# Kernel tuning notes

Measured on AMD Instinct MI355X. Metric: run time of the kernel, lower is better.

Reference implementation:

```python
import jax, jax.numpy as jnp
import numpy as np

EPS_BN = 1e-5
EPS_NORM = 1e-12
NUM_HEADS = 8


def _bn_relu(x):
    # BatchNorm2d in training mode with fresh params (gamma=1, beta=0), then ReLU.
    m = x.mean((0, 2, 3), keepdims=True)
    v = x.var((0, 2, 3), keepdims=True)  # biased variance, as PyTorch uses for normalization
    return jax.nn.relu((x - m) * jax.lax.rsqrt(v + EPS_BN))


def _conv3(x, w, groups=1):
    # 3x3 conv, stride 1, padding 1 (NCHW / OIHW)
    return jax.lax.conv_general_dilated(
        x, w, (1, 1), ((1, 1), (1, 1)),
        dimension_numbers=('NCHW', 'OIHW', 'NCHW'),
        feature_group_count=groups)


def _encoder(x, w1, w2, w3):
    # Conv1x1 -> BN -> ReLU -> Conv k2 s2 -> BN -> ReLU -> Conv1x1 -> BN -> ReLU
    x = _bn_relu(jnp.einsum('bihw,oi->bohw', x, w1))
    b, c, h, w = x.shape
    # k=2,s=2 conv as a reshape + einsum (non-overlapping 2x2 patches)
    x = _bn_relu(jnp.einsum('bchpwq,ocpq->bohw', x.reshape(b, c, h // 2, 2, w // 2, 2), w2))
    return _bn_relu(jnp.einsum('bihw,oi->bohw', x, w3))


def _decoder(x, w1, w2, w3):
    # ConvT1x1 -> BN -> ReLU -> ConvT k2 s2 -> BN -> ReLU -> ConvT1x1 -> BN -> ReLU
    x = _bn_relu(jnp.einsum('bihw,io->bohw', x, w1))
    # ConvTranspose k=2,s=2: each input pixel expands to a 2x2 block
    y = jnp.einsum('bihw,iopq->bohpwq', x, w2)
    b, o, h, p, w, q = y.shape
    x = _bn_relu(y.reshape(b, o, h * p, w * q))
    return _bn_relu(jnp.einsum('bihw,io->bohw', x, w3))


def _l2norm(x):
    # F.normalize(dim=-1) with eps=1e-12
    return x / jnp.maximum(jnp.linalg.norm(x, axis=-1, keepdims=True), EPS_NORM)


def setup_inputs() -> dict:
    key = jax.random.key(0)
    ks = jax.random.split(key, 13)
    B, C, H, W = 8, 256, 64, 64
    d = C // 4  # attention dim after self.divide

    def rn(k, shape, s=0.1):
        return jax.random.normal(k, shape, jnp.float32) * s

    return {
        'x': jax.random.normal(ks[0], (B, C, H, W), jnp.float32),
        'y': jax.random.normal(ks[1], (B, C, H, W), jnp.float32),
        'temperature': jnp.ones((NUM_HEADS, 1, 1), jnp.float32),
        'enc_w1': rn(ks[2], (d // 2, C)),
        'enc_w2': rn(ks[3], (d // 2, d // 2, 2, 2)),
        'enc_w3': rn(ks[4], (d, d // 2)),
        'kv_w': rn(ks[5], (2 * d, d)),
        'kv_dw_w': rn(ks[6], (2 * d, 1, 3, 3)),
        'q_w': rn(ks[7], (d, d)),
        'q_dw_w': rn(ks[8], (d, d, 3, 3)),
        'proj_w': rn(ks[9], (d, d)),
        'dec_w1': rn(ks[10], (d, 2 * d)),
        'dec_w2': rn(ks[11], (2 * d, 2 * d, 2, 2)),
        'dec_w3': rn(ks[12], (2 * d, 4 * d)),
    }


def reference(x, y, temperature, enc_w1, enc_w2, enc_w3, kv_w, kv_dw_w,
              q_w, q_dw_w, proj_w, dec_w1, dec_w2, dec_w3):
    # Shared freshly-built encoder applied to both x and y (same weights,
    # BN batch stats computed per call).
    x = _encoder(x, enc_w1, enc_w2, enc_w3)
    y = _encoder(y, enc_w1, enc_w2, enc_w3)
    b, c, h, w = x.shape  # c = 64, h = w = 32

    kv = _conv3(jnp.einsum('bihw,oi->bohw', x, kv_w), kv_dw_w, groups=2 * c)
    k, v = jnp.split(kv, 2, axis=1)
    q = _conv3(jnp.einsum('bihw,oi->bohw', y, q_w), q_dw_w)  # regular 3x3 conv

    ch = c // NUM_HEADS
    heads = lambda t: t.reshape(b, NUM_HEADS, ch, h * w)  # b head c (h w)
    q, k, v = heads(q), heads(k), heads(v)
    q = _l2norm(q)
    k = _l2norm(k)
    temp = temperature[None]  # [1, head, 1, 1]

    # Spatial attention: [b, head, hw, hw]
    attn_s = jax.nn.softmax(jnp.einsum('bhcn,bhcm->bhnm', q, k) * temp, axis=-1)
    out_s = jnp.einsum('bhcn,bhnm->bhcm', v, attn_s).reshape(b, c, h, w)
    out_s = jnp.einsum('bihw,oi->bohw', out_s, proj_w)

    # Channel attention: [b, head, c, c]
    attn_c = jax.nn.softmax(jnp.einsum('bhcn,bhdn->bhcd', q, k) * temp, axis=-1)
    out_c = jnp.einsum('bhcd,bhdn->bhcn', attn_c, v).reshape(b, c, h, w)
    out_c = jnp.einsum('bihw,oi->bohw', out_c, proj_w)

    return _decoder(out_s + out_c, dec_w1, dec_w2, dec_w3)
```

## Files before the change

kernel.cpp:

```cpp
#include <hip/hip_runtime.h>
#include <hip/hip_bf16.h>

#define EPS_BN 1e-5f

#define PIPE_FENCE() asm volatile("" ::: "memory")

template<int OT, bool HASBN, bool HASSTATS>
__global__ __launch_bounds__(256,2) void conv1x1_kernel(
    const float* __restrict__ in0, const float* __restrict__ in1,
    const float* __restrict__ w, float* __restrict__ out,
    const float* __restrict__ stIn, float* __restrict__ stOut,
    int I, int O, int P, int wio, int zsplit, float invN)
{
  __shared__ float wl[2048];
  __shared__ float bnm[256], bnr[256];
  int tid = threadIdx.x;
  int o0 = blockIdx.y*OT;
  int z  = blockIdx.z;
  int t  = (z >= zsplit) ? 1 : 0;
  int b  = t ? (z - zsplit) : z;
  const float* in = t ? in1 : in0;

  for(int idx=tid; idx<I*OT; idx+=256){
    int i = idx/OT, j = idx - i*OT;
    wl[idx] = wio ? w[(size_t)i*O + o0 + j] : w[(size_t)(o0+j)*I + i];
  }
  if(HASBN){
    for(int i=tid; i<I; i+=256){
      float s  = stIn[((size_t)t*I + i)*2];
      float s2 = stIn[((size_t)t*I + i)*2+1];
      float m  = s*invN;
      bnm[i] = m;
      bnr[i] = rsqrtf(s2*invN - m*m + EPS_BN);
    }
  }
  __syncthreads();

  int p4 = blockIdx.x*256 + tid;
  const float4* inb = (const float4*)(in + (size_t)b*I*P) + p4;
  int P4 = P >> 2;

  float acc[OT][4];
#pragma unroll
  for(int j=0;j<OT;j++){ acc[j][0]=acc[j][1]=acc[j][2]=acc[j][3]=0.f; }

  auto consume = [&](const float4* vv, int i0){
#pragma unroll
    for(int u=0;u<8;u++){
      float4 v = vv[u];
      if(HASBN){
        float m = bnm[i0+u], r = bnr[i0+u];
        v.x = fmaxf((v.x-m)*r, 0.f); v.y = fmaxf((v.y-m)*r, 0.f);
        v.z = fmaxf((v.z-m)*r, 0.f); v.w = fmaxf((v.w-m)*r, 0.f);
      }
      const float* wr = &wl[(i0+u)*OT];
#pragma unroll
      for(int j=0;j<OT;j++){
        float wv = wr[j];
        acc[j][0] = fmaf(wv, v.x, acc[j][0]);
        acc[j][1] = fmaf(wv, v.y, acc[j][1]);
        acc[j][2] = fmaf(wv, v.z, acc[j][2]);
        acc[j][3] = fmaf(wv, v.w, acc[j][3]);
      }
    }
  };

  float4 va[8], vb[8];
#pragma unroll
  for(int u=0;u<8;u++) va[u] = inb[(size_t)u*P4];
  PIPE_FENCE();

  for(int i0=0;i0<I;i0+=16){
#pragma unroll
    for(int u=0;u<8;u++) vb[u] = inb[(size_t)(i0+8+u)*P4];
    PIPE_FENCE();
    consume(va, i0);
    if(i0+16 < I){
#pragma unroll
      for(int u=0;u<8;u++) va[u] = inb[(size_t)(i0+16+u)*P4];
    }
    PIPE_FENCE();
    consume(vb, i0+8);
  }

  float4* ob = (float4*)(out + ((size_t)z*O + o0)*P) + p4;
#pragma unroll
  for(int j=0;j<OT;j++){
    float4 vv = {acc[j][0], acc[j][1], acc[j][2], acc[j][3]};
    ob[(size_t)j*P4] = vv;
  }

  if(HASSTATS){
#pragma unroll
    for(int j=0;j<OT;j++){
      float s  = acc[j][0]+acc[j][1]+acc[j][2]+acc[j][3];
      float s2 = acc[j][0]*acc[j][0]+acc[j][1]*acc[j][1]
               + acc[j][2]*acc[j][2]+acc[j][3]*acc[j][3];
      for(int off=32; off>0; off>>=1){
        s  += __shfl_down(s,  off, 64);
        s2 += __shfl_down(s2, off, 64);
      }
      if((tid & 63)==0){
        atomicAdd(&stOut[((size_t)t*O + o0 + j)*2],   s);
        atomicAdd(&stOut[((size_t)t*O + o0 + j)*2+1], s2);
      }
    }
  }
}

template<int OT, bool HASBN, bool HASSTATS>
__global__ __launch_bounds__(256) void conv1x1_small(
    const float* __restrict__ in0, const float* __restrict__ in1,
    const float* __restrict__ w, float* __restrict__ out,
    const float* __restrict__ stIn, float* __restrict__ stOut,
    int I, int O, int wio, int zsplit, float invN)
{
  __shared__ float wl[512];
  __shared__ float bnm[128], bnr[128];
  int tid = threadIdx.x;
  int z  = blockIdx.z;
  int t  = (z >= zsplit) ? 1 : 0;
  int b  = t ? (z - zsplit) : z;
  const float* in = t ? in1 : in0;
  int W2 = 2*OT;

  for(int idx=tid; idx<I*W2; idx+=256){
    int i = idx/W2, slot = idx - i*W2;
    int oabs = blockIdx.y*W2 + slot;
    wl[idx] = wio ? w[(size_t)i*O + oabs] : w[(size_t)oabs*I + i];
  }
  if(HASBN){
    for(int i=tid; i<I; i+=256){
      float s  = stIn[((size_t)t*I + i)*2];
      float s2 = stIn[((size_t)t*I + i)*2+1];
      float m  = s*invN;
      bnm[i] = m;
      bnr[i] = rsqrtf(s2*invN - m*m + EPS_BN);
    }
  }
  __syncthreads();

  int p4 = blockIdx.x*128 + (tid & 127);
  int os = tid >> 7;
  const float4* inb = (const float4*)(in + (size_t)b*I*1024) + p4;

  float acc[OT][4];
#pragma unroll
  for(int j=0;j<OT;j++){ acc[j][0]=acc[j][1]=acc[j][2]=acc[j][3]=0.f; }

  float4 vb[8];
  for(int i0=0;i0<I;i0+=8){
#pragma unroll
    for(int u=0;u<8;u++) vb[u] = inb[(size_t)(i0+u)*256];
    PIPE_FENCE();
#pragma unroll
    for(int u=0;u<8;u++){
      float4 v = vb[u];
      if(HASBN){
        float m = bnm[i0+u], r = bnr[i0+u];
        v.x = fmaxf((v.x-m)*r, 0.f); v.y = fmaxf((v.y-m)*r, 0.f);
        v.z = fmaxf((v.z-m)*r, 0.f); v.w = fmaxf((v.w-m)*r, 0.f);
      }
      const float* wr = &wl[(i0+u)*W2 + os*OT];
#pragma unroll
      for(int j=0;j<OT;j++){
        float wv = wr[j];
        acc[j][0] = fmaf(wv, v.x, acc[j][0]);
        acc[j][1] = fmaf(wv, v.y, acc[j][1]);
        acc[j][2] = fmaf(wv, v.z, acc[j][2]);
        acc[j][3] = fmaf(wv, v.w, acc[j][3]);
      }
    }
  }

  int obase = blockIdx.y*W2 + os*OT;
  float4* ob = (float4*)(out + ((size_t)z*O + obase)*1024) + p4;
#pragma unroll
  for(int j=0;j<OT;j++){
    float4 vv = {acc[j][0], acc[j][1], acc[j][2], acc[j][3]};
    ob[(size_t)j*256] = vv;
  }

  if(HASSTATS){
#pragma unroll
    for(int j=0;j<OT;j++){
      float s  = acc[j][0]+acc[j][1]+acc[j][2]+acc[j][3];
      float s2 = acc[j][0]*acc[j][0]+acc[j][1]*acc[j][1]
               + acc[j][2]*acc[j][2]+acc[j][3]*acc[j][3];
      for(int off=32; off>0; off>>=1){
        s  += __shfl_down(s,  off, 64);
        s2 += __shfl_down(s2, off, 64);
      }
      if((tid & 63)==0){
        atomicAdd(&stOut[((size_t)t*O + obase + j)*2],   s);
        atomicAdd(&stOut[((size_t)t*O + obase + j)*2+1], s2);
      }
    }
  }
}

__global__ __launch_bounds__(256) void conv2x2s2_bn_kernel(
    const float* __restrict__ in, const float* __restrict__ w,
    float* __restrict__ out, const float* __restrict__ stIn,
    float* __restrict__ stOut, float invN)
{
  __shared__ float wl[512];
  __shared__ float bnm[32], bnr[32];
  int tid = threadIdx.x;
  int o0 = blockIdx.x*4;
  int rq = blockIdx.y;
  int z  = blockIdx.z;
  int t  = z >> 3;

  for(int idx=tid; idx<512; idx+=256){
    int osub = idx>>7, ch=(idx>>2)&31, pq=idx&3;
    wl[idx] = w[(((size_t)(o0+osub)*32 + ch)*4) + pq];
  }
  if(tid < 32){
    float s  = stIn[((size_t)t*32 + tid)*2];
    float s2 = stIn[((size_t)t*32 + tid)*2+1];
    float m  = s*invN;
    bnm[tid] = m;
    bnr[tid] = rsqrtf(s2*invN - m*m + EPS_BN);
  }
  __syncthreads();

  int os   = tid >> 6;
  int slot = tid & 63;
  int h    = rq*8 + (slot>>3);
  int wg   = slot & 7;
  int cb   = wg*8;
  const float* wbase = &wl[os*128];
  const float* inz = in + (size_t)z*32*4096;

  float acc[4] = {0,0,0,0};
  float4 c0,c1,c2,c3, n0_,n1_,n2_,n3_;
  c0 = *(const float4*)(inz + (size_t)0*4096 + (2*h)*64 + cb);
  c1 = *(const float4*)(inz + (size_t)0*4096 + (2*h)*64 + cb + 4);
  c2 = *(const float4*)(inz + (size_t)0*4096 + (2*h+1)*64 + cb);
  c3 = *(const float4*)(inz + (size_t)0*4096 + (2*h+1)*64 + cb + 4);
  for(int ch=0; ch<32; ch++){
    if(ch < 31){
      n0_ = *(const float4*)(inz + (size_t)(ch+1)*4096 + (2*h)*64 + cb);
      n1_ = *(const float4*)(inz + (size_t)(ch+1)*4096 + (2*h)*64 + cb + 4);
      n2_ = *(const float4*)(inz + (size_t)(ch+1)*4096 + (2*h+1)*64 + cb);
      n3_ = *(const float4*)(inz + (size_t)(ch+1)*4096 + (2*h+1)*64 + cb + 4);
    }
    float m = bnm[ch], r = bnr[ch];
    float t0[8] = {c0.x,c0.y,c0.z,c0.w,c1.x,c1.y,c1.z,c1.w};
    float t1[8] = {c2.x,c2.y,c2.z,c2.w,c3.x,c3.y,c3.z,c3.w};
#pragma unroll
    for(int e=0;e<8;e++){
      t0[e] = fmaxf((t0[e]-m)*r, 0.f);
      t1[e] = fmaxf((t1[e]-m)*r, 0.f);
    }
    const float* wp = wbase + ch*4;
#pragma unroll
    for(int k=0;k<4;k++){
      acc[k] = fmaf(wp[0], t0[2*k],   acc[k]);
      acc[k] = fmaf(wp[1], t0[2*k+1], acc[k]);
      acc[k] = fmaf(wp[2], t1[2*k],   acc[k]);
      acc[k] = fmaf(wp[3], t1[2*k+1], acc[k]);
    }
    c0=n0_; c1=n1_; c2=n2_; c3=n3_;
  }

  float4 vv = {acc[0],acc[1],acc[2],acc[3]};
  *(float4*)(out + ((size_t)z*32 + o0+os)*1024 + h*32 + wg*4) = vv;

  float s  = acc[0]+acc[1]+acc[2]+acc[3];
  float s2 = acc[0]*acc[0]+acc[1]*acc[1]+acc[2]*acc[2]+acc[3]*acc[3];
  for(int off=32; off>0; off>>=1){
    s  += __shfl_down(s,  off, 64);
    s2 += __shfl_down(s2, off, 64);
  }
  if((tid & 63)==0){
    atomicAdd(&stOut[((size_t)t*32 + o0 + os)*2],   s);
    atomicAdd(&stOut[((size_t)t*32 + o0 + os)*2+1], s2);
  }
}

__global__ __launch_bounds__(256) void upsample2x2_bn_kernel(
    const float* __restrict__ in, const float* __restrict__ w,
    float* __restrict__ out, const float* __restrict__ stIn,
    float* __restrict__ stOut, float invN)
{
  __shared__ float wl[1024];
  __shared__ float bnm[128], bnr[128];
  int tid = threadIdx.x;
  int o0 = blockIdx.x*2;
  int b  = blockIdx.y;

  for(int idx=tid; idx<1024; idx+=256){
    int pq = idx & 3, r = idx >> 2;
    int i = r >> 1, j = r & 1;
    wl[idx] = w[((size_t)i*128 + o0+j)*4 + pq];
  }
  if(tid < 128){
    float s  = stIn[(size_t)tid*2];
    float s2 = stIn[(size_t)tid*2+1];
    float m  = s*invN;
    bnm[tid] = m;
    bnr[tid] = rsqrtf(s2*invN - m*m + EPS_BN);
  }
  __syncthreads();

  int h  = tid >> 3;
  int wg = tid & 7;
  int w0 = wg*4;

  float acc[2][16];
#pragma unroll
  for(int j=0;j<2;j++) for(int e=0;e<16;e++) acc[j][e]=0.f;

  float4 vb4[8];
  for(int i0=0;i0<128;i0+=8){
#pragma unroll
    for(int u=0;u<8;u++)
      vb4[u] = *(const float4*)(in + (((size_t)b*128+i0+u)*1024) + h*32 + w0);
    PIPE_FENCE();
#pragma unroll
    for(int u=0;u<8;u++){
      int i = i0+u;
      float4 v = vb4[u];
      float m = bnm[i], r = bnr[i];
      float vk[4] = {fmaxf((v.x-m)*r,0.f), fmaxf((v.y-m)*r,0.f),
                     fmaxf((v.z-m)*r,0.f), fmaxf((v.w-m)*r,0.f)};
#pragma unroll
      for(int j=0;j<2;j++){
        const float* wj = &wl[(i*2+j)*4];
#pragma unroll
        for(int pq=0;pq<4;pq++){
#pragma unroll
          for(int k=0;k<4;k++)
            acc[j][pq*4+k] = fmaf(wj[pq], vk[k], acc[j][pq*4+k]);
        }
      }
    }
  }

#pragma unroll
  for(int j=0;j<2;j++){
    float* ob = out + ((size_t)b*128 + o0+j)*4096;
#pragma unroll
    for(int p=0;p<2;p++){
      float4 A = {acc[j][(p*2+0)*4+0], acc[j][(p*2+1)*4+0],
                  acc[j][(p*2+0)*4+1], acc[j][(p*2+1)*4+1]};
      float4 B = {acc[j][(p*2+0)*4+2], acc[j][(p*2+1)*4+2],
                  acc[j][(p*2+0)*4+3], acc[j][(p*2+1)*4+3]};
      *(float4*)(ob + (2*h+p)*64 + 2*w0)     = A;
      *(float4*)(ob + (2*h+p)*64 + 2*w0 + 4) = B;
    }
  }

#pragma unroll
  for(int j=0;j<2;j++){
    float s=0.f, s2=0.f;
#pragma unroll
    for(int e=0;e<16;e++){ s += acc[j][e]; s2 += acc[j][e]*acc[j][e]; }
    for(int off=32; off>0; off>>=1){
      s  += __shfl_down(s,  off, 64);
      s2 += __shfl_down(s2, off, 64);
    }
    if((tid & 63)==0){
      atomicAdd(&stOut[((size_t)(o0+j))*2],   s);
      atomicAdd(&stOut[((size_t)(o0+j))*2+1], s2);
    }
  }
}

__global__ __launch_bounds__(256) void bn_final_kernel(
    float* __restrict__ x, const float* __restrict__ st, float invN)
{
  int idx4 = blockIdx.x*256 + threadIdx.x;
  int c = (idx4 >> 10) & 255;
  float s  = st[(size_t)c*2];
  float s2 = st[(size_t)c*2+1];
  float m  = s*invN;
  float r  = rsqrtf(s2*invN - m*m + EPS_BN);
  float4 v = ((float4*)x)[idx4];
  v.x = fmaxf((v.x-m)*r, 0.f); v.y = fmaxf((v.y-m)*r, 0.f);
  v.z = fmaxf((v.z-m)*r, 0.f); v.w = fmaxf((v.w-m)*r, 0.f);
  ((float4*)x)[idx4] = v;
}

__global__ __launch_bounds__(256) void dwconv3x3_kernel(
    const float* __restrict__ in, const float* __restrict__ w,
    float* __restrict__ out, int C)
{
  int c = blockIdx.x, b = blockIdx.y;
  int tid = threadIdx.x;
  __shared__ float wl[9];
  if(tid < 9) wl[tid] = w[c*9 + tid];
  __syncthreads();
  int h = tid >> 3, x4 = tid & 7;
  int c0 = x4*4;
  const float* base = in + ((size_t)b*C + c)*1024;
  float ax=0.f, ay=0.f, az=0.f, aw=0.f;
#pragma unroll
  for(int dr=0; dr<3; dr++){
    int r = h + dr - 1;
    if((unsigned)r >= 32u) continue;
    const float* row = base + r*32 + c0;
    float4 cc = *(const float4*)row;
    float l  = (x4>0) ? row[-1] : 0.f;
    float rr = (x4<7) ? row[4]  : 0.f;
    float w0=wl[dr*3], w1=wl[dr*3+1], w2=wl[dr*3+2];
    ax = fmaf(w0,l,   fmaf(w1,cc.x, fmaf(w2,cc.y, ax)));
    ay = fmaf(w0,cc.x,fmaf(w1,cc.y, fmaf(w2,cc.z, ay)));
    az = fmaf(w0,cc.y,fmaf(w1,cc.z, fmaf(w2,cc.w, az)));
    aw = fmaf(w0,cc.z,fmaf(w1,cc.w, fmaf(w2,rr,  aw)));
  }
  float4 vv = {ax,ay,az,aw};
  *(float4*)(out + ((size_t)b*C + c)*1024 + h*32 + c0) = vv;
}

__global__ __launch_bounds__(256) void conv3x3_kernel(
    const float* __restrict__ in, const float* __restrict__ w,
    float* __restrict__ out, int IC)
{
  int o = blockIdx.x, b = blockIdx.y;
  int tid = threadIdx.x;
  __shared__ float wl[576];
  for(int t=tid; t<IC*9; t+=256) wl[t] = w[(size_t)o*IC*9 + t];
  __syncthreads();
  int h = tid >> 3, x4 = tid & 7;
  int c0 = x4*4;
  const float* inb = in + (size_t)b*IC*1024;
  float ax=0.f, ay=0.f, az=0.f, aw=0.f;
#pragma unroll 2
  for(int i=0;i<IC;i++){
    const float* base = inb + (size_t)i*1024;
    const float* wp = &wl[i*9];
#pragma unroll
    for(int dr=0; dr<3; dr++){
      int r = h + dr - 1;
      if((unsigned)r >= 32u) continue;
      const float* row = base + r*32 + c0;
      float4 cc = *(const float4*)row;
      float l  = (x4>0) ? row[-1] : 0.f;
      float rr = (x4<7) ? row[4]  : 0.f;
      float w0=wp[dr*3], w1=wp[dr*3+1], w2=wp[dr*3+2];
      ax = fmaf(w0,l,   fmaf(w1,cc.x, fmaf(w2,cc.y, ax)));
      ay = fmaf(w0,cc.x,fmaf(w1,cc.y, fmaf(w2,cc.z, ay)));
      az = fmaf(w0,cc.y,fmaf(w1,cc.z, fmaf(w2,cc.w, az)));
      aw = fmaf(w0,cc.z,fmaf(w1,cc.w, fmaf(w2,rr,  aw)));
    }
  }
  float4 vv = {ax,ay,az,aw};
  *(float4*)(out + ((size_t)b*gridDim.x + o)*1024 + h*32 + c0) = vv;
}

__global__ __launch_bounds__(256) void norm_scale_kernel(
    const float* __restrict__ q, const float* __restrict__ kv,
    float* __restrict__ scl)
{
  int r = blockIdx.x;
  const float* p;
  if(r < 512){ int b=r>>6, c=r&63; p = q + ((size_t)b*64+c)*1024; }
  else { int rr=r-512; int b=rr>>6, c=rr&63; p = kv + ((size_t)b*128+c)*1024; }
  int tid = threadIdx.x;
  float4 v = ((const float4*)p)[tid];
  float s = v.x*v.x + v.y*v.y + v.z*v.z + v.w*v.w;
  __shared__ float ls[256];
  ls[tid]=s; __syncthreads();
  for(int st=128; st>0; st>>=1){ if(tid<st) ls[tid]+=ls[tid+st]; __syncthreads(); }
  if(tid==0) scl[r] = 1.f/fmaxf(sqrtf(ls[0]), 1e-12f);
}

__global__ __launch_bounds__(256) void attn_pass1(
    const float* __restrict__ q, const float* __restrict__ kv,
    const float* __restrict__ temp, const float* __restrict__ scl,
    float* __restrict__ den_out)
{
  int bx = blockIdx.x, hh = blockIdx.y, b = blockIdx.z;
  int nchunk = bx >> 2, mq = bx & 3;
  int tid = threadIdx.x;
  __shared__ __align__(16) float kl[256*12];
  const float* kb = kv + ((size_t)b*128 + hh*8)*1024 + mq*256;
  for(int t=tid;t<2048;t+=256){
    int c=t>>8, m=t&255;
    kl[m*12+c] = kb[(size_t)c*1024+m] * scl[512 + b*64 + hh*8 + c];
  }
  __syncthreads();
  int n = nchunk*256 + tid;
  const float* qp = q + ((size_t)b*64 + hh*8)*1024 + n;
  float th = temp[hh];
  float mxb = fabsf(th);
  float qr[8];
#pragma unroll
  for(int c=0;c<8;c++) qr[c] = qp[(size_t)c*1024] * scl[b*64+hh*8+c] * th;
  const float4* kl4 = (const float4*)kl;
  float den = 0.f, den2 = 0.f;
  for(int m=0;m<256;m+=2){
    float4 a  = kl4[m*3],     a2 = kl4[m*3+1];
    float4 bt = kl4[(m+1)*3], b2 = kl4[(m+1)*3+1];
    float s0 = qr[0]*a.x+qr[1]*a.y+qr[2]*a.z+qr[3]*a.w
             + qr[4]*a2.x+qr[5]*a2.y+qr[6]*a2.z+qr[7]*a2.w;
    float s1 = qr[0]*bt.x+qr[1]*bt.y+qr[2]*bt.z+qr[3]*bt.w
             + qr[4]*b2.x+qr[5]*b2.y+qr[6]*b2.z+qr[7]*b2.w;
    den  += __expf(s0 - mxb);
    den2 += __expf(s1 - mxb);
  }
  atomicAdd(&den_out[((size_t)(b*8+hh))*1024+n], den+den2);
}

__global__ __launch_bounds__(256) void attn_pass2(
    const float* __restrict__ q, const float* __restrict__ kv,
    const float* __restrict__ temp, const float* __restrict__ scl,
    const float* __restrict__ den, float* __restrict__ out)
{
  int bx = blockIdx.x, hh = blockIdx.y, b = blockIdx.z;
  int mchunk = bx >> 2, nq = bx & 3;
  int tid = threadIdx.x;
  __shared__ __align__(16) float ql[256*12];
  __shared__ __align__(16) float vl[256*12];
  __shared__ float idl[256];
  int bh = b*8+hh;
  int n0 = nq*256;
  const float* qb = q  + ((size_t)b*64 + hh*8)*1024 + n0;
  const float* vb = kv + ((size_t)b*128 + 64 + hh*8)*1024 + n0;
  for(int t=tid;t<2048;t+=256){
    int c=t>>8, n=t&255;
    ql[n*12+c] = qb[(size_t)c*1024+n] * scl[b*64+hh*8+c];
    vl[n*12+c] = vb[(size_t)c*1024+n];
  }
  idl[tid] = 1.f/den[(size_t)bh*1024 + n0 + tid];
  __syncthreads();
  int m = mchunk*256 + tid;
  const float* kb = kv + ((size_t)b*128 + hh*8)*1024 + m;
  float th = temp[hh];
  float mxb = fabsf(th);
  float kr[8];
#pragma unroll
  for(int c=0;c<8;c++) kr[c] = kb[(size_t)c*1024] * scl[512+b*64+hh*8+c] * th;
  float acc[8] = {0,0,0,0,0,0,0,0};
  const float4* ql4 = (const float4*)ql;
  const float4* vl4 = (const float4*)vl;
  for(int n=0;n<256;n+=2){
    float4 qa = ql4[n*3],     qa2 = ql4[n*3+1];
    float4 qc = ql4[(n+1)*3], qc2 = ql4[(n+1)*3+1];
    float s0 = kr[0]*qa.x+kr[1]*qa.y+kr[2]*qa.z+kr[3]*qa.w
             + kr[4]*qa2.x+kr[5]*qa2.y+kr[6]*qa2.z+kr[7]*qa2.w;
    float s1 = kr[0]*qc.x+kr[1]*qc.y+kr[2]*qc.z+kr[3]*qc.w
             + kr[4]*qc2.x+kr[5]*qc2.y+kr[6]*qc2.z+kr[7]*qc2.w;
    float p0 = __expf(s0 - mxb) * idl[n];
    float p1 = __expf(s1 - mxb) * idl[n+1];
    float4 va = vl4[n*3],     va2 = vl4[n*3+1];
    float4 vc = vl4[(n+1)*3], vc2 = vl4[(n+1)*3+1];
    acc[0]+=p0*va.x + p1*vc.x; acc[1]+=p0*va.y + p1*vc.y;
    acc[2]+=p0*va.z + p1*vc.z; acc[3]+=p0*va.w + p1*vc.w;
    acc[4]+=p0*va2.x + p1*vc2.x; acc[5]+=p0*va2.y + p1*vc2.y;
    acc[6]+=p0*va2.z + p1*vc2.z; acc[7]+=p0*va2.w + p1*vc2.w;
  }
  float* ob = out + ((size_t)b*64 + hh*8)*1024 + m;
#pragma unroll
  for(int c=0;c<8;c++) atomicAdd(&ob[(size_t)c*1024], acc[c]);
}

__global__ __launch_bounds__(256) void attn_channel(
    const float* __restrict__ q, const float* __restrict__ kv,
    const float* __restrict__ temp, const float* __restrict__ scl,
    float* out)
{
  int hh = blockIdx.x, b = blockIdx.y;
  __shared__ float kl[8192];
  const float* qb = q  + ((size_t)b*64 + hh*8)*1024;
  const float* kb = kv + ((size_t)b*128 + hh*8)*1024;
  const float* vb = kv + ((size_t)b*128 + 64 + hh*8)*1024;
  int tid = threadIdx.x;
  for(int t=tid;t<8192;t+=256) kl[t]=kb[t];
  __syncthreads();
  __shared__ float part[256];
  __shared__ float a[64];
  {
    int pair = tid >> 2, seg = tid & 3;
    int c = pair >> 3, d = pair & 7;
    const float* qrow = qb + (size_t)c*1024 + seg*256;
    const float* krow = kl + d*1024 + seg*256;
    float s = 0.f;
#pragma unroll 4
    for(int n=0;n<256;n++) s += qrow[n]*krow[n];
    part[tid] = s;
  }
  __syncthreads();
  if(tid < 64){
    int c = tid >> 3, d = tid & 7;
    float g = part[tid*4]+part[tid*4+1]+part[tid*4+2]+part[tid*4+3];
    part[tid] = g * scl[b*64+hh*8+c] * scl[512+b*64+hh*8+d] * temp[hh];
  }
  __syncthreads();
  if(tid < 8){
    float mx = -3.4e38f;
    for(int d=0;d<8;d++) mx = fmaxf(mx, part[tid*8+d]);
    float den = 0.f;
    float e[8];
    for(int d=0;d<8;d++){ e[d] = __expf(part[tid*8+d]-mx); den+=e[d]; }
    float inv = 1.f/den;
    for(int d=0;d<8;d++) a[tid*8+d] = e[d]*inv;
  }
  __syncthreads();
  float* ob = out + ((size_t)b*64 + hh*8)*1024;
  for(int n=tid;n<1024;n+=256){
    float vv[8];
#pragma unroll
    for(int d=0;d<8;d++) vv[d] = vb[(size_t)d*1024+n];
#pragma unroll
    for(int c=0;c<8;c++){
      float s = 0.f;
#pragma unroll
      for(int d=0;d<8;d++) s += a[c*8+d]*vv[d];
      ob[(size_t)c*1024+n] += s;
    }
  }
}

extern "C" void kernel_launch(void* const* d_in, const int* in_sizes, int n_in,
                              void* d_out, int out_size, void* d_ws, size_t ws_size,
                              hipStream_t stream)
{
  (void)in_sizes; (void)n_in; (void)out_size; (void)ws_size;
  const float* x      = (const float*)d_in[0];
  const float* y      = (const float*)d_in[1];
  const float* temp   = (const float*)d_in[2];
  const float* enc_w1 = (const float*)d_in[3];
  const float* enc_w2 = (const float*)d_in[4];
  const float* enc_w3 = (const float*)d_in[5];
  const float* kv_w   = (const float*)d_in[6];
  const float* kv_dw_w= (const float*)d_in[7];
  const float* q_w    = (const float*)d_in[8];
  const float* q_dw_w = (const float*)d_in[9];
  const float* proj_w = (const float*)d_in[10];
  const float* dec_w1 = (const float*)d_in[11];
  const float* dec_w2 = (const float*)d_in[12];
  const float* dec_w3 = (const float*)d_in[13];
  float* out = (float*)d_out;

  float* W   = (float*)d_ws;
  float* ST  = W;
  float* ST0 = ST;
  float* ST1 = ST + 128;
  float* ST2 = ST + 256;
  float* ST3 = ST + 512;
  float* ST4 = ST + 768;
  float* ST5 = ST + 1024;
  float* A    = W + 2048;
  float* E1   = A;
  float* KV1  = A;
  float* QPre = A + 1048576;
  float* ATTN = A;
  float* PROJ = A + 524288;
  float* D1   = A + 1048576;
  float* E2   = W + 2099200;
  float* E3   = W + 2623488;
  float* KV   = W + 3672064;
  float* Q    = W + 4720640;
  float* SCL  = W + 5244928;
  float* DEN  = W + 5245952;
  float* D2   = W + 2099200;

  const float inv32k = 1.f/32768.f, inv8k = 1.f/8192.f;

  hipMemsetAsync(ST, 0, 2048*sizeof(float), stream);
  hipMemsetAsync(DEN, 0, 65536*sizeof(float), stream);

  conv1x1_kernel<4,false,true><<<dim3(4,8,16),256,0,stream>>>(
      x, y, enc_w1, E1, nullptr, ST0, 256, 32, 4096, 0, 8, 0.f);
  conv2x2s2_bn_kernel<<<dim3(8,4,16),256,0,stream>>>(E1, enc_w2, E2, ST0, ST1, inv32k);
  conv1x1_small<1,true,true><<<dim3(2,32,16),256,0,stream>>>(
      E2, E2 + (size_t)8*32*1024, enc_w3, E3, ST1, ST2, 32, 64, 0, 8, inv8k);

  conv1x1_small<1,true,false><<<dim3(2,64,8),256,0,stream>>>(
      E3, E3, kv_w, KV1, ST2, nullptr, 64, 128, 0, 999, inv8k);
  dwconv3x3_kernel<<<dim3(128,8),256,0,stream>>>(KV1, kv_dw_w, KV, 128);
  conv1x1_small<1,true,false><<<dim3(2,32,8),256,0,stream>>>(
      E3 + (size_t)8*64*1024, E3, q_w, QPre, ST2 + 128, nullptr, 64, 64, 0, 999, inv8k);
  conv3x3_kernel<<<dim3(64,8),256,0,stream>>>(QPre, q_dw_w, Q, 64);

  hipMemsetAsync(ATTN, 0, 524288*sizeof(float), stream);

  norm_scale_kernel<<<1024,256,0,stream>>>(Q, KV, SCL);

  attn_pass1<<<dim3(16,8,8),256,0,stream>>>(Q, KV, temp, SCL, DEN);
  attn_pass2<<<dim3(16,8,8),256,0,stream>>>(Q, KV, temp, SCL, DEN, ATTN);
  attn_channel<<<dim3(8,8),256,0,stream>>>(Q, KV, temp, SCL, ATTN);

  conv1x1_small<1,false,false><<<dim3(2,32,8),256,0,stream>>>(
      ATTN, ATTN, proj_w, PROJ, nullptr, nullptr, 64, 64, 0, 999, 0.f);

  conv1x1_small<1,false,true><<<dim3(2,64,8),256,0,stream>>>(
      PROJ, PROJ, dec_w1, D1, nullptr, ST3, 64, 128, 1, 999, 0.f);
  upsample2x2_bn_kernel<<<dim3(64,8),256,0,stream>>>(D1, dec_w2, D2, ST3, ST4, inv8k);
  conv1x1_kernel<8,true,true><<<dim3(4,32,8),256,0,stream>>>(
      D2, D2, dec_w3, out, ST4, ST5, 128, 256, 4096, 1, 999, inv32k);
  bn_final_kernel<<<8192,256,0,stream>>>(out, ST5, inv32k);
}
```

Before: 586.3 us.

## Restructure 1x1 conv to one pixel per thread with wide output-channel tiles

Replaces the float4-per-thread conv1x1 kernel, which computed a few output channels per block, with a column variant. Each thread now handles one pixel and accumulates 32 or 64 output channels, reading weights from shared memory as float4. Every input element is read from global memory once per block instead of once per small group of output channels, which cuts redundant input traffic in the encoder's first conv and the decoder's last conv. BN statistics are reduced across waves in shared memory before the atomics, lowering atomic count. In exchange there are more accumulator registers per thread and fewer blocks in the grid.

```diff
diff --git a/kernel.cpp b/kernel.cpp
--- a/kernel.cpp
+++ b/kernel.cpp
@@ -5,25 +5,32 @@
 
 #define PIPE_FENCE() asm volatile("" ::: "memory")
 
-template<int OT, bool HASBN, bool HASSTATS>
-__global__ __launch_bounds__(256,2) void conv1x1_kernel(
+template<int OS, bool HASBN, bool HASSTATS>
+__global__ __launch_bounds__(256,2) void conv1x1_col(
     const float* __restrict__ in0, const float* __restrict__ in1,
     const float* __restrict__ w, float* __restrict__ out,
     const float* __restrict__ stIn, float* __restrict__ stOut,
     int I, int O, int P, int wio, int zsplit, float invN)
 {
-  __shared__ float wl[2048];
+  __shared__ __align__(16) float wl[8192];
   __shared__ float bnm[256], bnr[256];
   int tid = threadIdx.x;
-  int o0 = blockIdx.y*OT;
-  int z  = blockIdx.z;
-  int t  = (z >= zsplit) ? 1 : 0;
-  int b  = t ? (z - zsplit) : z;
+  int z = blockIdx.z;
+  int t = (z >= zsplit) ? 1 : 0;
+  int b = t ? (z - zsplit) : z;
   const float* in = t ? in1 : in0;
-
-  for(int idx=tid; idx<I*OT; idx+=256){
-    int i = idx/OT, j = idx - i*OT;
-    wl[idx] = wio ? w[(size_t)i*O + o0 + j] : w[(size_t)(o0+j)*I + i];
+  int o0 = blockIdx.y*OS;
+
+  if(wio){
+    for(int idx=tid; idx<I*OS; idx+=256){
+      int i = idx/OS, oo = idx - i*OS;
+      wl[idx] = w[(size_t)i*O + o0 + oo];
+    }
+  } else {
+    for(int idx=tid; idx<I*OS; idx+=256){
+      int oo = idx/I, i = idx - oo*I;
+      wl[i*OS + oo] = w[(size_t)(o0+oo)*I + i];
+    }
   }
   if(HASBN){
     for(int i=tid; i<I; i+=256){
@@ -36,74 +43,90 @@
   }
   __syncthreads();
 
-  int p4 = blockIdx.x*256 + tid;
-  const float4* inb = (const float4*)(in + (size_t)b*I*P) + p4;
-  int P4 = P >> 2;
-
-  float acc[OT][4];
-#pragma unroll
-  for(int j=0;j<OT;j++){ acc[j][0]=acc[j][1]=acc[j][2]=acc[j][3]=0.f; }
-
-  auto consume = [&](const float4* vv, int i0){
-#pragma unroll
-    for(int u=0;u<8;u++){
-      float4 v = vv[u];
-      if(HASBN){
-        float m = bnm[i0+u], r = bnr[i0+u];
-        v.x = fmaxf((v.x-m)*r, 0.f); v.y = fmaxf((v.y-m)*r, 0.f);
-        v.z = fmaxf((v.z-m)*r, 0.f); v.w = fmaxf((v.w-m)*r, 0.f);
-      }
-      const float* wr = &wl[(i0+u)*OT];
-#pragma unroll
-      for(int j=0;j<OT;j++){
-        float wv = wr[j];
-        acc[j][0] = fmaf(wv, v.x, acc[j][0]);
-        acc[j][1] = fmaf(wv, v.y, acc[j][1]);
-        acc[j][2] = fmaf(wv, v.z, acc[j][2]);
-        acc[j][3] = fmaf(wv, v.w, acc[j][3]);
-      }
-    }
-  };
-
-  float4 va[8], vb[8];
-#pragma unroll
-  for(int u=0;u<8;u++) va[u] = inb[(size_t)u*P4];
+  int p = blockIdx.x*256 + tid;
+  const float* inp = in + (size_t)b*I*P + p;
+
+  float acc[OS];
+#pragma unroll
+  for(int j=0;j<OS;j++) acc[j]=0.f;
+
+  float va[16], vb[16];
+#pragma unroll
+  for(int u=0;u<16;u++) va[u] = inp[(size_t)u*P];
   PIPE_FENCE();
 
-  for(int i0=0;i0<I;i0+=16){
-#pragma unroll
-    for(int u=0;u<8;u++) vb[u] = inb[(size_t)(i0+8+u)*P4];
+  for(int i0=0; i0<I; i0+=32){
+#pragma unroll
+    for(int u=0;u<16;u++) vb[u] = inp[(size_t)(i0+16+u)*P];
     PIPE_FENCE();
-    consume(va, i0);
-    if(i0+16 < I){
-#pragma unroll
-      for(int u=0;u<8;u++) va[u] = inb[(size_t)(i0+16+u)*P4];
+#pragma unroll
+    for(int u=0;u<16;u++){
+      float v = va[u];
+      if(HASBN){ int i=i0+u; v = fmaxf((v-bnm[i])*bnr[i], 0.f); }
+      const float4* wr4 = (const float4*)&wl[(i0+u)*OS];
+#pragma unroll
+      for(int q=0;q<OS/4;q++){
+        float4 wq = wr4[q];
+        acc[q*4+0] = fmaf(wq.x, v, acc[q*4+0]);
+        acc[q*4+1] = fmaf(wq.y, v, acc[q*4+1]);
+        acc[q*4+2] = fmaf(wq.z, v, acc[q*4+2]);
+        acc[q*4+3] = fmaf(wq.w, v, acc[q*4+3]);
+      }
+    }
+    if(i0+32 < I){
+#pragma unroll
+      for(int u=0;u<16;u++) va[u] = inp[(size_t)(i0+32+u)*P];
     }
     PIPE_FENCE();
-    consume(vb, i0+8);
-  }
-
-  float4* ob = (float4*)(out + ((size_t)z*O + o0)*P) + p4;
-#pragma unroll
-  for(int j=0;j<OT;j++){
-    float4 vv = {acc[j][0], acc[j][1], acc[j][2], acc[j][3]};
-    ob[(size_t)j*P4] = vv;
-  }
+#pragma unroll
+    for(int u=0;u<16;u++){
+      float v = vb[u];
+      if(HASBN){ int i=i0+16+u; v = fmaxf((v-bnm[i])*bnr[i], 0.f); }
+      const float4* wr4 = (const float4*)&wl[(i0+16+u)*OS];
+#pragma unroll
+      for(int q=0;q<OS/4;q++){
+        float4 wq = wr4[q];
+        acc[q*4+0] = fmaf(wq.x, v, acc[q*4+0]);
+        acc[q*4+1] = fmaf(wq.y, v, acc[q*4+1]);
+        acc[q*4+2] = fmaf(wq.z, v, acc[q*4+2]);
+        acc[q*4+3] = fmaf(wq.w, v, acc[q*4+3]);
+      }
+    }
+    PIPE_FENCE();
+  }
+
+  float* ob = out + (size_t)z*O*P + p;
+#pragma unroll
+  for(int j=0;j<OS;j++) ob[(size_t)(o0+j)*P] = acc[j];
 
   if(HASSTATS){
-#pragma unroll
-    for(int j=0;j<OT;j++){
-      float s  = acc[j][0]+acc[j][1]+acc[j][2]+acc[j][3];
-      float s2 = acc[j][0]*acc[j][0]+acc[j][1]*acc[j][1]
-               + acc[j][2]*acc[j][2]+acc[j][3]*acc[j][3];
+    int wid  = tid >> 6;
+    float ws[OS], ws2[OS];
+#pragma unroll
+    for(int j=0;j<OS;j++){
+      float s = acc[j], s2 = acc[j]*acc[j];
       for(int off=32; off>0; off>>=1){
         s  += __shfl_down(s,  off, 64);
         s2 += __shfl_down(s2, off, 64);
       }
-      if((tid & 63)==0){
-        atomicAdd(&stOut[((size_t)t*O + o0 + j)*2],   s);
-        atomicAdd(&stOut[((size_t)t*O + o0 + j)*2+1], s2);
-      }
+      ws[j]=s; ws2[j]=s2;
+    }
+    __syncthreads();
+    if((tid & 63)==0){
+#pragma unroll
+      for(int j=0;j<OS;j++){
+        wl[(wid*OS + j)*2]   = ws[j];
+        wl[(wid*OS + j)*2+1] = ws2[j];
+      }
+    }
+    __syncthreads();
+    if(tid < OS){
+      float s  = wl[tid*2]         + wl[(OS+tid)*2]
+               + wl[(2*OS+tid)*2]  + wl[(3*OS+tid)*2];
+      float s2 = wl[tid*2+1]       + wl[(OS+tid)*2+1]
+               + wl[(2*OS+tid)*2+1]+ wl[(3*OS+tid)*2+1];
+      atomicAdd(&stOut[((size_t)t*O + o0 + tid)*2],   s);
+      atomicAdd(&stOut[((size_t)t*O + o0 + tid)*2+1], s2);
     }
   }
 }
@@ -664,7 +687,7 @@
   hipMemsetAsync(ST, 0, 2048*sizeof(float), stream);
   hipMemsetAsync(DEN, 0, 65536*sizeof(float), stream);
 
-  conv1x1_kernel<4,false,true><<<dim3(4,8,16),256,0,stream>>>(
+  conv1x1_col<32,false,true><<<dim3(16,1,16),256,0,stream>>>(
       x, y, enc_w1, E1, nullptr, ST0, 256, 32, 4096, 0, 8, 0.f);
   conv2x2s2_bn_kernel<<<dim3(8,4,16),256,0,stream>>>(E1, enc_w2, E2, ST0, ST1, inv32k);
   conv1x1_small<1,true,true><<<dim3(2,32,16),256,0,stream>>>(
@@ -691,7 +714,7 @@
   conv1x1_small<1,false,true><<<dim3(2,64,8),256,0,stream>>>(
       PROJ, PROJ, dec_w1, D1, nullptr, ST3, 64, 128, 1, 999, 0.f);
   upsample2x2_bn_kernel<<<dim3(64,8),256,0,stream>>>(D1, dec_w2, D2, ST3, ST4, inv8k);
-  conv1x1_kernel<8,true,true><<<dim3(4,32,8),256,0,stream>>>(
+  conv1x1_col<64,true,true><<<dim3(16,4,8),256,0,stream>>>(
       D2, D2, dec_w3, out, ST4, ST5, 128, 256, 4096, 1, 999, inv32k);
   bn_final_kernel<<<8192,256,0,stream>>>(out, ST5, inv32k);
 }
```

Measured after the change: 1.833 ms. 213% more time.

## Enlarge output tiles in 1x1 convs and swizzle block order across XCDs

Applied to the files above, without the earlier changes.

The generic 1x1 conv kernel gets a configurable prefetch depth and a 1D grid with optional XCD-aware block remapping, so each batch's blocks stay on one XCD. The encoder's first conv now computes 8 output channels per block instead of 4, halving how often the 256-channel input is reread. The decoder's last conv computes 16 per block instead of 8, with a shallower prefetch depth. The aim is less redundant global reads and better L2 locality, at the cost of more accumulator registers, which may spill or lower occupancy.

```diff
diff --git a/kernel.cpp b/kernel.cpp
--- a/kernel.cpp
+++ b/kernel.cpp
@@ -5,18 +5,31 @@
 
 #define PIPE_FENCE() asm volatile("" ::: "memory")
 
-template<int OT, bool HASBN, bool HASSTATS>
+template<int OT, int D, bool HASBN, bool HASSTATS>
 __global__ __launch_bounds__(256,2) void conv1x1_kernel(
     const float* __restrict__ in0, const float* __restrict__ in1,
     const float* __restrict__ w, float* __restrict__ out,
     const float* __restrict__ stIn, float* __restrict__ stOut,
-    int I, int O, int P, int wio, int zsplit, float invN)
+    int I, int O, int P, int wio, int zsplit, float invN,
+    int nx, int ny, int swz)
 {
   __shared__ float wl[2048];
   __shared__ float bnm[256], bnr[256];
   int tid = threadIdx.x;
-  int o0 = blockIdx.y*OT;
-  int z  = blockIdx.z;
+
+  int bid = blockIdx.x;
+  int nb  = nx*ny;
+  int xb, yb, z;
+  if(swz){
+    int xcd = bid & 7, slot = bid >> 3;
+    int zl = slot/nb, inner = slot - zl*nb;
+    xb = inner % nx; yb = inner / nx; z = xcd + 8*zl;
+  } else {
+    int zq = bid / nb, inner = bid - zq*nb;
+    xb = inner % nx; yb = inner / nx; z = zq;
+  }
+
+  int o0 = yb*OT;
   int t  = (z >= zsplit) ? 1 : 0;
   int b  = t ? (z - zsplit) : z;
   const float* in = t ? in1 : in0;
@@ -36,7 +49,7 @@
   }
   __syncthreads();
 
-  int p4 = blockIdx.x*256 + tid;
+  int p4 = xb*256 + tid;
   const float4* inb = (const float4*)(in + (size_t)b*I*P) + p4;
   int P4 = P >> 2;
 
@@ -46,7 +59,7 @@
 
   auto consume = [&](const float4* vv, int i0){
 #pragma unroll
-    for(int u=0;u<8;u++){
+    for(int u=0;u<D;u++){
       float4 v = vv[u];
       if(HASBN){
         float m = bnm[i0+u], r = bnr[i0+u];
@@ -65,22 +78,22 @@
     }
   };
 
-  float4 va[8], vb[8];
-#pragma unroll
-  for(int u=0;u<8;u++) va[u] = inb[(size_t)u*P4];
+  float4 va[D], vb[D];
+#pragma unroll
+  for(int u=0;u<D;u++) va[u] = inb[(size_t)u*P4];
   PIPE_FENCE();
 
-  for(int i0=0;i0<I;i0+=16){
-#pragma unroll
-    for(int u=0;u<8;u++) vb[u] = inb[(size_t)(i0+8+u)*P4];
+  for(int i0=0;i0<I;i0+=2*D){
+#pragma unroll
+    for(int u=0;u<D;u++) vb[u] = inb[(size_t)(i0+D+u)*P4];
     PIPE_FENCE();
     consume(va, i0);
-    if(i0+16 < I){
-#pragma unroll
-      for(int u=0;u<8;u++) va[u] = inb[(size_t)(i0+16+u)*P4];
+    if(i0+2*D < I){
+#pragma unroll
+      for(int u=0;u<D;u++) va[u] = inb[(size_t)(i0+2*D+u)*P4];
     }
     PIPE_FENCE();
-    consume(vb, i0+8);
+    consume(vb, i0+D);
   }
 
   float4* ob = (float4*)(out + ((size_t)z*O + o0)*P) + p4;
@@ -664,8 +677,9 @@
   hipMemsetAsync(ST, 0, 2048*sizeof(float), stream);
   hipMemsetAsync(DEN, 0, 65536*sizeof(float), stream);
 
-  conv1x1_kernel<4,false,true><<<dim3(4,8,16),256,0,stream>>>(
-      x, y, enc_w1, E1, nullptr, ST0, 256, 32, 4096, 0, 8, 0.f);
+  conv1x1_kernel<8,8,false,true><<<256,256,0,stream>>>(
+      x, y, enc_w1, E1, nullptr, ST0, 256, 32, 4096, 0, 8, 0.f,
+      4, 4, 1);
   conv2x2s2_bn_kernel<<<dim3(8,4,16),256,0,stream>>>(E1, enc_w2, E2, ST0, ST1, inv32k);
   conv1x1_small<1,true,true><<<dim3(2,32,16),256,0,stream>>>(
       E2, E2 + (size_t)8*32*1024, enc_w3, E3, ST1, ST2, 32, 64, 0, 8, inv8k);
@@ -691,7 +705,8 @@
   conv1x1_small<1,false,true><<<dim3(2,64,8),256,0,stream>>>(
       PROJ, PROJ, dec_w1, D1, nullptr, ST3, 64, 128, 1, 999, 0.f);
   upsample2x2_bn_kernel<<<dim3(64,8),256,0,stream>>>(D1, dec_w2, D2, ST3, ST4, inv8k);
-  conv1x1_kernel<8,true,true><<<dim3(4,32,8),256,0,stream>>>(
-      D2, D2, dec_w3, out, ST4, ST5, 128, 256, 4096, 1, 999, inv32k);
+  conv1x1_kernel<16,4,true,true><<<512,256,0,stream>>>(
+      D2, D2, dec_w3, out, ST4, ST5, 128, 256, 4096, 1, 999, inv32k,
+      4, 16, 0);
   bn_final_kernel<<<8192,256,0,stream>>>(out, ST5, inv32k);
 }
```

Result: no change. 579.1 us (-1.2%).
